# Performance work log

Hardware: AMD Instinct MI355X
Metric: run time of the kernel (lower is better)

Reference implementation:

```python
import jax, jax.numpy as jnp
import numpy as np

M, N, D, P = 16, 4096, 128, 8192
H = N // D


def setup_inputs() -> dict:
    key = jax.random.key(0)
    ks = jax.random.split(key, 6)
    s = 1.0 / np.sqrt(N)
    return {
        "X": jax.random.normal(ks[0], (M, N), dtype=jnp.float32),
        "W_q": jax.random.normal(ks[1], (N, N), dtype=jnp.float32) * s,
        "W_k": jax.random.normal(ks[2], (N, N), dtype=jnp.float32) * s,
        "W_v": jax.random.normal(ks[3], (N, N), dtype=jnp.float32) * s,
        "cache_K": jax.random.normal(ks[4], (H, P, D), dtype=jnp.float32),
        "cache_V": jax.random.normal(ks[5], (H, P, D), dtype=jnp.float32),
    }


def reference(X, W_q, W_k, W_v, cache_K, cache_V):
    m = X.shape[0]
    h, p, d = cache_K.shape
    # QKV projections: [M, N] @ [N, N] -> [M, H, D] -> [H, M, D]
    q = (X @ W_q).reshape(m, h, d).transpose(1, 0, 2)
    k = (X @ W_k).reshape(m, h, d).transpose(1, 0, 2)
    v = (X @ W_v).reshape(m, h, d).transpose(1, 0, 2)
    # KV-cache concat along the sequence axis -> [H, P+M, D]
    k_all = jnp.concatenate([cache_K, k], axis=1)
    v_all = jnp.concatenate([cache_V, v], axis=1)
    # attention (note: original applies NO 1/sqrt(D) scaling)
    scores = jnp.einsum('hmd,hpd->hmp', q, k_all)  # [H, M, P+M]
    weights = jax.nn.softmax(scores, axis=-1)
    out = jnp.einsum('hmp,hpd->hmd', weights, v_all)  # [H, M, D]
    return out.transpose(1, 0, 2).reshape(m, h * d)
```

## Files before the change

### kernel.cpp

```cpp
#include <hip/hip_runtime.h>

#define HN 32
#define MM 16
#define DD 128
#define NN 4096
#define PP 8192
#define TP 32
#define NCH 48
#define CLEN 171
#define NTILE 6

__global__ __launch_bounds__(256) void qkv_kernel(
    const float* __restrict__ X, const float* __restrict__ Wq,
    const float* __restrict__ Wk, const float* __restrict__ Wv,
    float* __restrict__ qkv)
{
    __shared__ float Xs[MM][128];
    const int bx  = blockIdx.x;
    const int mat = bx >> 8;
    const int r   = bx & 255;
    const int ct  = r >> 5;
    const int rc  = r & 31;
    const int col0 = ct << 9;
    const int i0   = rc << 7;
    const float* W = (mat == 0) ? Wq : (mat == 1) ? Wk : Wv;
    const int t = threadIdx.x;

    for (int f = t; f < MM*128; f += 256)
        Xs[f >> 7][f & 127] = X[(f >> 7)*NN + i0 + (f & 127)];
    __syncthreads();

    const int c0 = col0 + t, c1 = col0 + 256 + t;
    float a0[MM], a1[MM];
#pragma unroll
    for (int m = 0; m < MM; ++m) { a0[m] = 0.f; a1[m] = 0.f; }

    for (int i16 = 0; i16 < 128; i16 += 16) {
        const float* Wr = W + (size_t)(i0 + i16) * NN;
        float w0[16], w1[16];
#pragma unroll
        for (int rr = 0; rr < 16; ++rr) {
            w0[rr] = Wr[(size_t)rr*NN + c0];
            w1[rr] = Wr[(size_t)rr*NN + c1];
        }
#pragma unroll
        for (int m = 0; m < MM; ++m) {
            float4 xa = *reinterpret_cast<const float4*>(&Xs[m][i16]);
            float4 xb = *reinterpret_cast<const float4*>(&Xs[m][i16 + 4]);
            float4 xc = *reinterpret_cast<const float4*>(&Xs[m][i16 + 8]);
            float4 xd = *reinterpret_cast<const float4*>(&Xs[m][i16 + 12]);
            a0[m] += xa.x*w0[0] + xa.y*w0[1] + xa.z*w0[2] + xa.w*w0[3]
                   + xb.x*w0[4] + xb.y*w0[5] + xb.z*w0[6] + xb.w*w0[7]
                   + xc.x*w0[8] + xc.y*w0[9] + xc.z*w0[10] + xc.w*w0[11]
                   + xd.x*w0[12] + xd.y*w0[13] + xd.z*w0[14] + xd.w*w0[15];
            a1[m] += xa.x*w1[0] + xa.y*w1[1] + xa.z*w1[2] + xa.w*w1[3]
                   + xb.x*w1[4] + xb.y*w1[5] + xb.z*w1[6] + xb.w*w1[7]
                   + xc.x*w1[8] + xc.y*w1[9] + xc.z*w1[10] + xc.w*w1[11]
                   + xd.x*w1[12] + xd.y*w1[13] + xd.z*w1[14] + xd.w*w1[15];
        }
    }
    float* base = qkv + (size_t)mat * HN*MM*DD;
    const int h0 = c0 >> 7, d0 = c0 & 127;
    const int h1 = c1 >> 7, d1 = c1 & 127;
#pragma unroll
    for (int m = 0; m < MM; ++m) {
        atomicAdd(&base[(h0*MM + m)*DD + d0], a0[m]);
        atomicAdd(&base[(h1*MM + m)*DD + d1], a1[m]);
    }
}

__global__ __launch_bounds__(256, 2) void attn_partial5(
    const float* __restrict__ cacheK, const float* __restrict__ cacheV,
    const float* __restrict__ qkv, float* __restrict__ pmu,
    float* __restrict__ ps, float* __restrict__ pacc)
{
    __shared__ float KV[TP][DD + 4];
    __shared__ float Wl[TP][20];

    const int chunk = blockIdx.x;
    const int h     = blockIdx.y;
    const int t     = threadIdx.x;
    const int lane  = t & 63;
    const int wv    = __builtin_amdgcn_readfirstlane((int)(threadIdx.x >> 6));
    const int hf    = lane >> 5;
    const int p     = lane & 31;
    const int srow  = t >> 3;
    const int sg    = t & 7;
    const int psi   = lane >> 4;
    const int g     = lane & 15;

    const float* k_ws = qkv + HN*MM*DD;
    const float* v_ws = qkv + 2*HN*MM*DD;
    const int start = chunk * CLEN;
    const float* qA = qkv + ((size_t)h*MM + 4*wv + 2*hf)*DD;
    const float* qB = qA + DD;

    float mu0 = -3.0e38f, mu1 = -3.0e38f, mu2 = -3.0e38f, mu3 = -3.0e38f;
    float ss0 = 0.f, ss1 = 0.f, ss2 = 0.f, ss3 = 0.f;
    float acc[4][8];
#pragma unroll
    for (int q = 0; q < 4; ++q)
#pragma unroll
        for (int k = 0; k < 8; ++k) acc[q][k] = 0.f;

    for (int tt = 0; tt < NTILE; ++tt) {
        const int valid = min(TP, CLEN - tt*TP);
        const int vr    = min(start + tt*TP + srow, PP + MM - 1);
        const float* srcK = (vr < PP) ? cacheK + ((size_t)h*PP + vr)*DD
                                      : k_ws + ((size_t)h*MM + (vr - PP))*DD;
        const float* srcV = (vr < PP) ? cacheV + ((size_t)h*PP + vr)*DD
                                      : v_ws + ((size_t)h*MM + (vr - PP))*DD;

        __syncthreads();
        {
            float4 k0 = *reinterpret_cast<const float4*>(srcK + 4*sg);
            float4 k1 = *reinterpret_cast<const float4*>(srcK + 4*sg + 32);
            float4 k2 = *reinterpret_cast<const float4*>(srcK + 4*sg + 64);
            float4 k3 = *reinterpret_cast<const float4*>(srcK + 4*sg + 96);
            *reinterpret_cast<float4*>(&KV[srow][4*sg])      = k0;
            *reinterpret_cast<float4*>(&KV[srow][4*sg + 32]) = k1;
            *reinterpret_cast<float4*>(&KV[srow][4*sg + 64]) = k2;
            *reinterpret_cast<float4*>(&KV[srow][4*sg + 96]) = k3;
        }
        __syncthreads();

        float sA = 0.f, sB = 0.f;
#pragma unroll 8
        for (int dq = 0; dq < 32; ++dq) {
            float4 k = *reinterpret_cast<const float4*>(&KV[p][dq*4]);
            float4 a = *reinterpret_cast<const float4*>(qA + dq*4);
            float4 b = *reinterpret_cast<const float4*>(qB + dq*4);
            sA += k.x*a.x + k.y*a.y + k.z*a.z + k.w*a.w;
            sB += k.x*b.x + k.y*b.y + k.z*b.z + k.w*b.w;
        }
        if (p >= valid) { sA = -3.0e38f; sB = -3.0e38f; }

        __syncthreads();
        {
            float4 v0 = *reinterpret_cast<const float4*>(srcV + 4*sg);
            float4 v1 = *reinterpret_cast<const float4*>(srcV + 4*sg + 32);
            float4 v2 = *reinterpret_cast<const float4*>(srcV + 4*sg + 64);
            float4 v3 = *reinterpret_cast<const float4*>(srcV + 4*sg + 96);
            *reinterpret_cast<float4*>(&KV[srow][4*sg])      = v0;
            *reinterpret_cast<float4*>(&KV[srow][4*sg + 32]) = v1;
            *reinterpret_cast<float4*>(&KV[srow][4*sg + 64]) = v2;
            *reinterpret_cast<float4*>(&KV[srow][4*sg + 96]) = v3;
        }

        float mA = sA, mB = sB;
#pragma unroll
        for (int off = 1; off < 32; off <<= 1) {
            mA = fmaxf(mA, __shfl_xor(mA, off));
            mB = fmaxf(mB, __shfl_xor(mB, off));
        }
        const float mAo = __shfl_xor(mA, 32), mBo = __shfl_xor(mB, 32);
        const float m0 = hf ? mAo : mA, m1 = hf ? mBo : mB;
        const float m2 = hf ? mA : mAo, m3 = hf ? mB : mBo;
        const float n0 = fmaxf(mu0, m0), n1 = fmaxf(mu1, m1);
        const float n2 = fmaxf(mu2, m2), n3 = fmaxf(mu3, m3);
        const float r0 = __expf(mu0 - n0), r1 = __expf(mu1 - n1);
        const float r2 = __expf(mu2 - n2), r3 = __expf(mu3 - n3);
        const float wA = __expf(sA - (hf ? n2 : n0));
        const float wB = __expf(sB - (hf ? n3 : n1));
        float tA = wA, tB = wB;
#pragma unroll
        for (int off = 1; off < 32; off <<= 1) {
            tA += __shfl_xor(tA, off);
            tB += __shfl_xor(tB, off);
        }
        const float tAo = __shfl_xor(tA, 32), tBo = __shfl_xor(tB, 32);
        ss0 = ss0*r0 + (hf ? tAo : tA);
        ss1 = ss1*r1 + (hf ? tBo : tB);
        ss2 = ss2*r2 + (hf ? tA : tAo);
        ss3 = ss3*r3 + (hf ? tB : tBo);
        mu0 = n0; mu1 = n1; mu2 = n2; mu3 = n3;
        *reinterpret_cast<float2*>(&Wl[p][4*wv + 2*hf]) = make_float2(wA, wB);

        __syncthreads();

#pragma unroll
        for (int k = 0; k < 8; ++k) {
            acc[0][k] *= r0; acc[1][k] *= r1; acc[2][k] *= r2; acc[3][k] *= r3;
        }
#pragma unroll
        for (int i = 0; i < 8; ++i) {
            const int pp = psi + 4*i;
            float4 wq = *reinterpret_cast<const float4*>(&Wl[pp][4*wv]);
            float4 v0 = *reinterpret_cast<const float4*>(&KV[pp][g*8]);
            float4 v1 = *reinterpret_cast<const float4*>(&KV[pp][g*8 + 4]);
            acc[0][0] += wq.x*v0.x; acc[0][1] += wq.x*v0.y; acc[0][2] += wq.x*v0.z; acc[0][3] += wq.x*v0.w;
            acc[0][4] += wq.x*v1.x; acc[0][5] += wq.x*v1.y; acc[0][6] += wq.x*v1.z; acc[0][7] += wq.x*v1.w;
            acc[1][0] += wq.y*v0.x; acc[1][1] += wq.y*v0.y; acc[1][2] += wq.y*v0.z; acc[1][3] += wq.y*v0.w;
            acc[1][4] += wq.y*v1.x; acc[1][5] += wq.y*v1.y; acc[1][6] += wq.y*v1.z; acc[1][7] += wq.y*v1.w;
            acc[2][0] += wq.z*v0.x; acc[2][1] += wq.z*v0.y; acc[2][2] += wq.z*v0.z; acc[2][3] += wq.z*v0.w;
            acc[2][4] += wq.z*v1.x; acc[2][5] += wq.z*v1.y; acc[2][6] += wq.z*v1.z; acc[2][7] += wq.z*v1.w;
            acc[3][0] += wq.w*v0.x; acc[3][1] += wq.w*v0.y; acc[3][2] += wq.w*v0.z; acc[3][3] += wq.w*v0.w;
            acc[3][4] += wq.w*v1.x; acc[3][5] += wq.w*v1.y; acc[3][6] += wq.w*v1.z; acc[3][7] += wq.w*v1.w;
        }
    }

#pragma unroll
    for (int q = 0; q < 4; ++q)
#pragma unroll
        for (int k = 0; k < 8; ++k) {
            float v = acc[q][k];
            v += __shfl_xor(v, 16);
            v += __shfl_xor(v, 32);
            acc[q][k] = v;
        }
    if (lane < 16) {
        float* pa = pacc + ((size_t)(h*NCH + chunk)*MM + 4*wv)*DD;
#pragma unroll
        for (int q = 0; q < 4; ++q) {
            *reinterpret_cast<float4*>(pa + q*DD + g*8) =
                make_float4(acc[q][0], acc[q][1], acc[q][2], acc[q][3]);
            *reinterpret_cast<float4*>(pa + q*DD + g*8 + 4) =
                make_float4(acc[q][4], acc[q][5], acc[q][6], acc[q][7]);
        }
    }
    if (lane == 0) {
        const int o = (h*NCH + chunk)*MM + 4*wv;
        pmu[o + 0] = mu0; pmu[o + 1] = mu1; pmu[o + 2] = mu2; pmu[o + 3] = mu3;
        ps [o + 0] = ss0; ps [o + 1] = ss1; ps [o + 2] = ss2; ss3 = ss3;
        ps [o + 3] = ss3; ps [o + 2] = ss2;
    }
}

__global__ __launch_bounds__(128) void combine_kernel(
    const float* __restrict__ pmu, const float* __restrict__ ps,
    const float* __restrict__ pacc, float* __restrict__ out)
{
    const int b = blockIdx.x;
    const int h = b >> 4, m = b & 15;
    const int d = threadIdx.x;
    float gm = -3.0e38f;
#pragma unroll 8
    for (int c = 0; c < NCH; ++c)
        gm = fmaxf(gm, pmu[(h*NCH + c)*MM + m]);
    float stot = 0.f, a = 0.f;
#pragma unroll 8
    for (int c = 0; c < NCH; ++c) {
        const float f = __expf(pmu[(h*NCH + c)*MM + m] - gm);
        stot += ps[(h*NCH + c)*MM + m] * f;
        a += pacc[((size_t)(h*NCH + c)*MM + m)*DD + d] * f;
    }
    out[m*NN + h*DD + d] = a / stot;
}

extern "C" void kernel_launch(void* const* d_in, const int* in_sizes, int n_in,
                              void* d_out, int out_size, void* d_ws, size_t ws_size,
                              hipStream_t stream) {
    const float* X  = (const float*)d_in[0];
    const float* Wq = (const float*)d_in[1];
    const float* Wk = (const float*)d_in[2];
    const float* Wv = (const float*)d_in[3];
    const float* cK = (const float*)d_in[4];
    const float* cV = (const float*)d_in[5];
    float* out = (float*)d_out;

    float* ws     = (float*)d_ws;
    float* qkv    = ws;
    float* pmu_p  = ws + 3*HN*MM*DD;
    float* ps_p   = pmu_p + HN*NCH*MM;
    float* pacc_p = ps_p + HN*NCH*MM;

    hipMemsetAsync(qkv, 0, (size_t)3*HN*MM*DD*sizeof(float), stream);
    qkv_kernel<<<768, 256, 0, stream>>>(X, Wq, Wk, Wv, qkv);
    attn_partial5<<<dim3(NCH, HN), 256, 0, stream>>>(cK, cV, qkv, pmu_p, ps_p, pacc_p);
    combine_kernel<<<HN*MM, 128, 0, stream>>>(pmu_p, ps_p, pacc_p, out);
}
```

Before: 206.5 us.

## Double-buffer K tiles via direct global-to-LDS loads, read V from global

Rewrites the attention partial kernel so K tiles are prefetched into a double-buffered, XOR-swizzled LDS buffer using global_load_lds. The next tile's load overlaps compute on the current one. V is now read directly from global memory instead of being staged through shared memory, which removes several barriers per tile. Chunking changes to 32 aligned 256-row chunks, with the new tokens handled as a tail tile in the last chunk. The trade-offs are fewer blocks (1024 vs 1536) and uncoalesced-ish per-thread V global reads, plus a load imbalance on the last chunk.

New measurement: 206.3 us. No clear change (-0.1%).

```diff
diff --git a/kernel.cpp b/kernel.cpp
--- a/kernel.cpp
+++ b/kernel.cpp
@@ -6,9 +6,14 @@
 #define NN 4096
 #define PP 8192
 #define TP 32
-#define NCH 48
-#define CLEN 171
-#define NTILE 6
+#define NCH 32
+#define CROWS 256
+
+__device__ __forceinline__ void gll16(const void* g, void* l) {
+    __builtin_amdgcn_global_load_lds(
+        (const __attribute__((address_space(1))) void*)g,
+        (__attribute__((address_space(3))) void*)l, 16, 0, 0);
+}
 
 __global__ __launch_bounds__(256) void qkv_kernel(
     const float* __restrict__ X, const float* __restrict__ Wq,
@@ -69,12 +74,12 @@
     }
 }
 
-__global__ __launch_bounds__(256, 2) void attn_partial5(
+__global__ __launch_bounds__(256, 2) void attn_partial8(
     const float* __restrict__ cacheK, const float* __restrict__ cacheV,
     const float* __restrict__ qkv, float* __restrict__ pmu,
     float* __restrict__ ps, float* __restrict__ pacc)
 {
-    __shared__ float KV[TP][DD + 4];
+    __shared__ float Ks[2][TP*DD];
     __shared__ float Wl[TP][20];
 
     const int chunk = blockIdx.x;
@@ -84,16 +89,18 @@
     const int wv    = __builtin_amdgcn_readfirstlane((int)(threadIdx.x >> 6));
     const int hf    = lane >> 5;
     const int p     = lane & 31;
-    const int srow  = t >> 3;
-    const int sg    = t & 7;
     const int psi   = lane >> 4;
     const int g     = lane & 15;
 
     const float* k_ws = qkv + HN*MM*DD;
     const float* v_ws = qkv + 2*HN*MM*DD;
-    const int start = chunk * CLEN;
+    const float* Kbase = cacheK + ((size_t)h*PP + (size_t)chunk*CROWS)*DD;
+    const float* Vbase = cacheV + ((size_t)h*PP + (size_t)chunk*CROWS)*DD;
     const float* qA = qkv + ((size_t)h*MM + 4*wv + 2*hf)*DD;
     const float* qB = qA + DD;
+
+    const int nfull = CROWS / TP;
+    const int ntile = nfull + (chunk == NCH - 1 ? 1 : 0);
 
     float mu0 = -3.0e38f, mu1 = -3.0e38f, mu2 = -3.0e38f, mu3 = -3.0e38f;
     float ss0 = 0.f, ss1 = 0.f, ss2 = 0.f, ss3 = 0.f;
@@ -103,49 +110,55 @@
 #pragma unroll
         for (int k = 0; k < 8; ++k) acc[q][k] = 0.f;
 
-    for (int tt = 0; tt < NTILE; ++tt) {
-        const int valid = min(TP, CLEN - tt*TP);
-        const int vr    = min(start + tt*TP + srow, PP + MM - 1);
-        const float* srcK = (vr < PP) ? cacheK + ((size_t)h*PP + vr)*DD
-                                      : k_ws + ((size_t)h*MM + (vr - PP))*DD;
-        const float* srcV = (vr < PP) ? cacheV + ((size_t)h*PP + vr)*DD
-                                      : v_ws + ((size_t)h*MM + (vr - PP))*DD;
-
-        __syncthreads();
-        {
-            float4 k0 = *reinterpret_cast<const float4*>(srcK + 4*sg);
-            float4 k1 = *reinterpret_cast<const float4*>(srcK + 4*sg + 32);
-            float4 k2 = *reinterpret_cast<const float4*>(srcK + 4*sg + 64);
-            float4 k3 = *reinterpret_cast<const float4*>(srcK + 4*sg + 96);
-            *reinterpret_cast<float4*>(&KV[srow][4*sg])      = k0;
-            *reinterpret_cast<float4*>(&KV[srow][4*sg + 32]) = k1;
-            *reinterpret_cast<float4*>(&KV[srow][4*sg + 64]) = k2;
-            *reinterpret_cast<float4*>(&KV[srow][4*sg + 96]) = k3;
-        }
-        __syncthreads();
+#pragma unroll
+    for (int i = 0; i < 4; ++i) {
+        const int seg = wv*4 + i;
+        const int row = 2*seg + (lane >> 5);
+        const int c   = (lane & 31) ^ (row & 7);
+        gll16(Kbase + (size_t)row*DD + 4*c, &Ks[0][seg*256]);
+    }
+    asm volatile("s_waitcnt vmcnt(0)" ::: "memory");
+    __syncthreads();
+
+    for (int tt = 0; tt < ntile; ++tt) {
+        const int  cur   = tt & 1;
+        const bool tail  = (tt == nfull);
+        const int  valid = tail ? MM : TP;
+        const float* KC  = &Ks[cur][0];
+
+        if (tt + 1 < ntile) {
+            float* KN = &Ks[cur ^ 1][0];
+            if (tt + 1 < nfull) {
+                const float* src = Kbase + (size_t)(tt + 1)*TP*DD;
+#pragma unroll
+                for (int i = 0; i < 4; ++i) {
+                    const int seg = wv*4 + i;
+                    const int row = 2*seg + (lane >> 5);
+                    const int c   = (lane & 31) ^ (row & 7);
+                    gll16(src + (size_t)row*DD + 4*c, KN + seg*256);
+                }
+            } else {
+                const float* src = k_ws + (size_t)h*MM*DD;
+#pragma unroll
+                for (int i = 0; i < 2; ++i) {
+                    const int seg = wv*2 + i;
+                    const int row = 2*seg + (lane >> 5);
+                    const int c   = (lane & 31) ^ (row & 7);
+                    gll16(src + (size_t)row*DD + 4*c, KN + seg*256);
+                }
+            }
+        }
 
         float sA = 0.f, sB = 0.f;
 #pragma unroll 8
         for (int dq = 0; dq < 32; ++dq) {
-            float4 k = *reinterpret_cast<const float4*>(&KV[p][dq*4]);
+            float4 k = *reinterpret_cast<const float4*>(KC + p*DD + ((dq ^ (p & 7)) << 2));
             float4 a = *reinterpret_cast<const float4*>(qA + dq*4);
             float4 b = *reinterpret_cast<const float4*>(qB + dq*4);
             sA += k.x*a.x + k.y*a.y + k.z*a.z + k.w*a.w;
             sB += k.x*b.x + k.y*b.y + k.z*b.z + k.w*b.w;
         }
         if (p >= valid) { sA = -3.0e38f; sB = -3.0e38f; }
-
-        __syncthreads();
-        {
-            float4 v0 = *reinterpret_cast<const float4*>(srcV + 4*sg);
-            float4 v1 = *reinterpret_cast<const float4*>(srcV + 4*sg + 32);
-            float4 v2 = *reinterpret_cast<const float4*>(srcV + 4*sg + 64);
-            float4 v3 = *reinterpret_cast<const float4*>(srcV + 4*sg + 96);
-            *reinterpret_cast<float4*>(&KV[srow][4*sg])      = v0;
-            *reinterpret_cast<float4*>(&KV[srow][4*sg + 32]) = v1;
-            *reinterpret_cast<float4*>(&KV[srow][4*sg + 64]) = v2;
-            *reinterpret_cast<float4*>(&KV[srow][4*sg + 96]) = v3;
-        }
 
         float mA = sA, mB = sB;
 #pragma unroll
@@ -176,18 +189,20 @@
         mu0 = n0; mu1 = n1; mu2 = n2; mu3 = n3;
         *reinterpret_cast<float2*>(&Wl[p][4*wv + 2*hf]) = make_float2(wA, wB);
 
-        __syncthreads();
-
 #pragma unroll
         for (int k = 0; k < 8; ++k) {
             acc[0][k] *= r0; acc[1][k] *= r1; acc[2][k] *= r2; acc[3][k] *= r3;
         }
-#pragma unroll
+        const float* srcV = tail ? v_ws + (size_t)h*MM*DD
+                                 : Vbase + (size_t)tt*TP*DD;
+#pragma unroll 4
         for (int i = 0; i < 8; ++i) {
-            const int pp = psi + 4*i;
+            const int pp   = psi + 4*i;
+            const int srcr = tail ? min(pp, MM - 1) : pp;
+            const float* vp = srcV + (size_t)srcr*DD + g*8;
             float4 wq = *reinterpret_cast<const float4*>(&Wl[pp][4*wv]);
-            float4 v0 = *reinterpret_cast<const float4*>(&KV[pp][g*8]);
-            float4 v1 = *reinterpret_cast<const float4*>(&KV[pp][g*8 + 4]);
+            float4 v0 = *reinterpret_cast<const float4*>(vp);
+            float4 v1 = *reinterpret_cast<const float4*>(vp + 4);
             acc[0][0] += wq.x*v0.x; acc[0][1] += wq.x*v0.y; acc[0][2] += wq.x*v0.z; acc[0][3] += wq.x*v0.w;
             acc[0][4] += wq.x*v1.x; acc[0][5] += wq.x*v1.y; acc[0][6] += wq.x*v1.z; acc[0][7] += wq.x*v1.w;
             acc[1][0] += wq.y*v0.x; acc[1][1] += wq.y*v0.y; acc[1][2] += wq.y*v0.z; acc[1][3] += wq.y*v0.w;
@@ -197,6 +212,9 @@
             acc[3][0] += wq.w*v0.x; acc[3][1] += wq.w*v0.y; acc[3][2] += wq.w*v0.z; acc[3][3] += wq.w*v0.w;
             acc[3][4] += wq.w*v1.x; acc[3][5] += wq.w*v1.y; acc[3][6] += wq.w*v1.z; acc[3][7] += wq.w*v1.w;
         }
+
+        asm volatile("s_waitcnt vmcnt(0)" ::: "memory");
+        __syncthreads();
     }
 
 #pragma unroll
@@ -221,8 +239,7 @@
     if (lane == 0) {
         const int o = (h*NCH + chunk)*MM + 4*wv;
         pmu[o + 0] = mu0; pmu[o + 1] = mu1; pmu[o + 2] = mu2; pmu[o + 3] = mu3;
-        ps [o + 0] = ss0; ps [o + 1] = ss1; ps [o + 2] = ss2; ss3 = ss3;
-        ps [o + 3] = ss3; ps [o + 2] = ss2;
+        ps [o + 0] = ss0; ps [o + 1] = ss1; ps [o + 2] = ss2; ps [o + 3] = ss3;
     }
 }
 
@@ -266,6 +283,6 @@
 
     hipMemsetAsync(qkv, 0, (size_t)3*HN*MM*DD*sizeof(float), stream);
     qkv_kernel<<<768, 256, 0, stream>>>(X, Wq, Wk, Wv, qkv);
-    attn_partial5<<<dim3(NCH, HN), 256, 0, stream>>>(cK, cV, qkv, pmu_p, ps_p, pacc_p);
+    attn_partial8<<<dim3(NCH, HN), 256, 0, stream>>>(cK, cV, qkv, pmu_p, ps_p, pacc_p);
     combine_kernel<<<HN*MM, 128, 0, stream>>>(pmu_p, ps_p, pacc_p, out);
 }
```
